# Performance work log

Measured on AMD Instinct MI355X. Metric: run time of the kernel, lower is better.

The kernel has to match this reference:

```python
import jax, jax.numpy as jnp
import numpy as np

EMBED_DIM = 1024

def setup_inputs() -> dict:
    key = jax.random.key(0)
    ks = jax.random.split(key, 7)
    D = EMBED_DIM
    x = jax.random.normal(ks[0], (4, 2048, D), dtype=jnp.float32)
    s = 1.0 / np.sqrt(D)
    Wq = jax.random.normal(ks[1], (D, D), dtype=jnp.float32) * s
    bq = jnp.zeros((D,), dtype=jnp.float32)
    Wk = jax.random.normal(ks[2], (D, D), dtype=jnp.float32) * s
    bk = jnp.zeros((D,), dtype=jnp.float32)
    Wv = jax.random.normal(ks[3], (D, D), dtype=jnp.float32) * s
    bv = jnp.zeros((D,), dtype=jnp.float32)
    return {"x": x, "Wq": Wq, "bq": bq, "Wk": Wk, "bk": bk, "Wv": Wv, "bv": bv}

def reference(x, Wq, bq, Wk, bk, Wv, bv):
    # x: [B,S,D]; torch Linear: x @ W.T + b -> here W is stored as [D_in, D_out]
    Q = jnp.einsum('bsd,de->bse', x, Wq) + bq
    K = jnp.einsum('bsd,de->bse', x, Wk) + bk
    V = jnp.einsum('bsd,de->bse', x, Wv) + bv
    scale = 1.0 / jnp.sqrt(jnp.asarray(x.shape[-1], dtype=x.dtype))
    scores = jnp.einsum('bqd,bkd->bqk', Q, K) * scale  # [B,S,S]
    probs = jax.nn.softmax(scores, axis=-1)
    # dropout is identity in eval mode
    return jnp.einsum('bqk,bkd->bqd', probs, V)
```

## Files before the change

### kernel.cpp

```cpp
#include <hip/hip_runtime.h>
#include <hip/hip_bf16.h>
#include <stdint.h>
#include <stddef.h>

#define D_EMB 1024
#define SEQ   2048
#define BATCH 4

typedef short bf16x8 __attribute__((ext_vector_type(8)));
typedef float f32x4  __attribute__((ext_vector_type(4)));

#define AS1 __attribute__((address_space(1)))
#define AS3 __attribute__((address_space(3)))

static __device__ __forceinline__ void async_copy16(const void* g, void* l) {
  __builtin_amdgcn_global_load_lds((const AS1 void*)g, (AS3 void*)l, 16, 0, 0);
}

static __device__ __forceinline__ void gemm128(
    const __hip_bfloat16* __restrict__ A, int lda,
    const __hip_bfloat16* __restrict__ Bt, int ldb,
    int K, f32x4 (&acc)[4][4])
{
  __shared__ __hip_bfloat16 ldsA[128 * 64];
  __shared__ __hip_bfloat16 ldsB[128 * 64];

  const int t    = threadIdx.x;
  const int wave = t >> 6;
  const int lane = t & 63;
  const int quad = lane >> 4;
  const int lr   = lane & 15;
  const int wr   = wave >> 1;
  const int wc   = wave & 1;

  const int r0 = t >> 3;
  const int c0 = (((t & 7) ^ (r0 & 7)) * 8);

  const __hip_bfloat16* gA = A  + (size_t)r0 * lda + c0;
  const __hip_bfloat16* gB = Bt + (size_t)r0 * ldb + c0;
  char* lA = (char*)ldsA + wave * 1024;
  char* lB = (char*)ldsB + wave * 1024;

  for (int k0 = 0; k0 < K; k0 += 64) {
    __syncthreads();
#pragma unroll
    for (int ch = 0; ch < 4; ch++) {
      async_copy16(gA + k0 + (size_t)(32 * ch) * lda, lA + 4096 * ch);
      async_copy16(gB + k0 + (size_t)(32 * ch) * ldb, lB + 4096 * ch);
    }
    __syncthreads();

#pragma unroll
    for (int kk = 0; kk < 64; kk += 32) {
      bf16x8 aF[4], bF[4];
      const int lc = (kk >> 3) + quad;
      const int pc = (lc ^ (lr & 7)) * 8;
#pragma unroll
      for (int i = 0; i < 4; i++)
        aF[i] = *(const bf16x8*)&ldsA[(wr * 64 + i * 16 + lr) * 64 + pc];
#pragma unroll
      for (int j = 0; j < 4; j++)
        bF[j] = *(const bf16x8*)&ldsB[(wc * 64 + j * 16 + lr) * 64 + pc];

#pragma unroll
      for (int i = 0; i < 4; i++)
#pragma unroll
        for (int j = 0; j < 4; j++)
          acc[i][j] = __builtin_amdgcn_mfma_f32_16x16x32_bf16(aF[i], bF[j], acc[i][j], 0, 0, 0);
    }
  }
}

#define ZERO_ACC(acc)                         \
  {                                           \
    f32x4 _z = {0.f, 0.f, 0.f, 0.f};          \
    _Pragma("unroll")                         \
    for (int _i = 0; _i < 4; _i++)            \
      _Pragma("unroll")                       \
      for (int _j = 0; _j < 4; _j++)          \
        acc[_i][_j] = _z;                     \
  }

__global__ __launch_bounds__(256) void convert_x(
    const float* __restrict__ x, __hip_bfloat16* __restrict__ xb)
{
  const size_t i = ((size_t)blockIdx.x * 256 + threadIdx.x) * 4;
  const float4 v = *(const float4*)(x + i);
  __hip_bfloat16 o[4] = {__float2bfloat16(v.x), __float2bfloat16(v.y),
                         __float2bfloat16(v.z), __float2bfloat16(v.w)};
  *(uint64_t*)(xb + i) = *(uint64_t*)o;
}

__global__ __launch_bounds__(256) void transpose_w3(
    const float* __restrict__ Wq,
    const float* __restrict__ Wk,
    const float* __restrict__ Wv,
    __hip_bfloat16* __restrict__ Wt3)
{
  const float* src = (blockIdx.z == 0) ? Wq : (blockIdx.z == 1) ? Wk : Wv;
  __hip_bfloat16* dst = Wt3 + (size_t)blockIdx.z * D_EMB * D_EMB;
  __shared__ __hip_bfloat16 tile[32][33];
  const int x0 = blockIdx.x * 32;
  const int y0 = blockIdx.y * 32;
  const int tx = threadIdx.x, ty = threadIdx.y;
#pragma unroll
  for (int i = 0; i < 32; i += 8)
    tile[ty + i][tx] = __float2bfloat16(src[(size_t)(y0 + ty + i) * D_EMB + (x0 + tx)]);
  __syncthreads();
#pragma unroll
  for (int i = 0; i < 32; i += 8)
    dst[(size_t)(x0 + ty + i) * D_EMB + (y0 + tx)] = tile[tx][ty + i];
}

__global__ __launch_bounds__(256) void qkv_kernel(
    const __hip_bfloat16* __restrict__ xb,
    const __hip_bfloat16* __restrict__ Wt3,
    const float* __restrict__ bq,
    const float* __restrict__ bk,
    const float* __restrict__ bv,
    __hip_bfloat16* __restrict__ Q,
    __hip_bfloat16* __restrict__ Kb,
    __hip_bfloat16* __restrict__ Vt)
{
  const int mat = blockIdx.z;
  const int m0  = blockIdx.x * 128;
  const int n0  = blockIdx.y * 128;

  f32x4 acc[4][4];
  ZERO_ACC(acc);

  gemm128(xb + (size_t)m0 * D_EMB, D_EMB,
          Wt3 + (size_t)mat * D_EMB * D_EMB + (size_t)n0 * D_EMB, D_EMB,
          D_EMB, acc);

  const float* bias = (mat == 0) ? bq : (mat == 1) ? bk : bv;

  const int t = threadIdx.x;
  const int wave = t >> 6, lane = t & 63;
  const int quad = lane >> 4, lr = lane & 15;
  const int wr = wave >> 1, wc = wave & 1;

#pragma unroll
  for (int i = 0; i < 4; i++) {
#pragma unroll
    for (int j = 0; j < 4; j++) {
      const int n = n0 + wc * 64 + j * 16 + lr;
      const float bb = bias[n];
#pragma unroll
      for (int r = 0; r < 4; r++) {
        const int m = m0 + wr * 64 + i * 16 + quad * 4 + r;
        const float v = acc[i][j][r] + bb;
        if (mat == 0) {
          Q[(size_t)m * D_EMB + n] = __float2bfloat16(v);
        } else if (mat == 1) {
          Kb[(size_t)m * D_EMB + n] = __float2bfloat16(v);
        } else {
          const int b = m >> 11, s = m & 2047;
          Vt[(size_t)b * D_EMB * SEQ + (size_t)n * SEQ + s] = __float2bfloat16(v);
        }
      }
    }
  }
}

__global__ __launch_bounds__(256) void scores_kernel(
    const __hip_bfloat16* __restrict__ Q,
    const __hip_bfloat16* __restrict__ Kb,
    float* __restrict__ Sc)
{
  const int b  = blockIdx.z;
  const int m0 = blockIdx.y * 128;
  const int n0 = blockIdx.x * 128;

  f32x4 acc[4][4];
  ZERO_ACC(acc);

  gemm128(Q  + (size_t)b * SEQ * D_EMB + (size_t)m0 * D_EMB, D_EMB,
          Kb + (size_t)b * SEQ * D_EMB + (size_t)n0 * D_EMB, D_EMB,
          D_EMB, acc);

  float* out = Sc + (size_t)b * SEQ * SEQ;
  const float scale = 0.03125f;

  const int t = threadIdx.x;
  const int wave = t >> 6, lane = t & 63;
  const int quad = lane >> 4, lr = lane & 15;
  const int wr = wave >> 1, wc = wave & 1;

#pragma unroll
  for (int i = 0; i < 4; i++)
#pragma unroll
    for (int j = 0; j < 4; j++) {
      const int n = n0 + wc * 64 + j * 16 + lr;
#pragma unroll
      for (int r = 0; r < 4; r++) {
        const int m = m0 + wr * 64 + i * 16 + quad * 4 + r;
        out[(size_t)m * SEQ + n] = acc[i][j][r] * scale;
      }
    }
}

__global__ __launch_bounds__(256) void softmax_kernel(
    const float* __restrict__ Sc, __hip_bfloat16* __restrict__ P)
{
  const int row = blockIdx.x;
  const float* src = Sc + (size_t)row * SEQ;
  const int t = threadIdx.x;
  const int wave = t >> 6, lane = t & 63;

  float v[8];
#pragma unroll
  for (int i = 0; i < 8; i++) v[i] = src[t + 256 * i];

  float m = v[0];
#pragma unroll
  for (int i = 1; i < 8; i++) m = fmaxf(m, v[i]);
#pragma unroll
  for (int o = 32; o > 0; o >>= 1) m = fmaxf(m, __shfl_xor(m, o));

  __shared__ float redm[4];
  __shared__ float reds[4];
  if (lane == 0) redm[wave] = m;
  __syncthreads();
  m = fmaxf(fmaxf(redm[0], redm[1]), fmaxf(redm[2], redm[3]));

  float e[8], s = 0.f;
#pragma unroll
  for (int i = 0; i < 8; i++) { e[i] = __expf(v[i] - m); s += e[i]; }
#pragma unroll
  for (int o = 32; o > 0; o >>= 1) s += __shfl_xor(s, o);
  if (lane == 0) reds[wave] = s;
  __syncthreads();
  s = reds[0] + reds[1] + reds[2] + reds[3];

  const float inv = 1.f / s;
  __hip_bfloat16* dst = P + (size_t)row * SEQ;
#pragma unroll
  for (int i = 0; i < 8; i++) dst[t + 256 * i] = __float2bfloat16(e[i] * inv);
}

__global__ __launch_bounds__(256) void pv_kernel(
    const __hip_bfloat16* __restrict__ P,
    const __hip_bfloat16* __restrict__ Vt,
    float* __restrict__ out)
{
  const int b  = blockIdx.z;
  const int m0 = blockIdx.y * 128;
  const int n0 = blockIdx.x * 128;

  f32x4 acc[4][4];
  ZERO_ACC(acc);

  gemm128(P  + (size_t)b * SEQ * SEQ   + (size_t)m0 * SEQ, SEQ,
          Vt + (size_t)b * D_EMB * SEQ + (size_t)n0 * SEQ, SEQ,
          SEQ, acc);

  float* o = out + (size_t)b * SEQ * D_EMB;

  const int t = threadIdx.x;
  const int wave = t >> 6, lane = t & 63;
  const int quad = lane >> 4, lr = lane & 15;
  const int wr = wave >> 1, wc = wave & 1;

#pragma unroll
  for (int i = 0; i < 4; i++)
#pragma unroll
    for (int j = 0; j < 4; j++) {
      const int n = n0 + wc * 64 + j * 16 + lr;
#pragma unroll
      for (int r = 0; r < 4; r++) {
        const int m = m0 + wr * 64 + i * 16 + quad * 4 + r;
        o[(size_t)m * D_EMB + n] = acc[i][j][r];
      }
    }
}

extern "C" void kernel_launch(void* const* d_in, const int* in_sizes, int n_in,
                              void* d_out, int out_size, void* d_ws, size_t ws_size,
                              hipStream_t stream) {
  const float* x  = (const float*)d_in[0];
  const float* Wq = (const float*)d_in[1];
  const float* bq = (const float*)d_in[2];
  const float* Wk = (const float*)d_in[3];
  const float* bk = (const float*)d_in[4];
  const float* Wv = (const float*)d_in[5];
  const float* bv = (const float*)d_in[6];
  float* out = (float*)d_out;

  char* ws = (char*)d_ws;
  __hip_bfloat16* xb  = (__hip_bfloat16*)(ws);
  __hip_bfloat16* Wt3 = (__hip_bfloat16*)(ws + 16777216);
  __hip_bfloat16* Q   = (__hip_bfloat16*)(ws + 23068672);
  __hip_bfloat16* Kb  = (__hip_bfloat16*)(ws + 39845888);
  __hip_bfloat16* Vt  = (__hip_bfloat16*)(ws + 56623104);
  float*          Sc  = (float*)         (ws + 73400320);
  __hip_bfloat16* P   = (__hip_bfloat16*)(ws + 140509184);

  convert_x    <<<dim3(8192),      256,        0, stream>>>(x, xb);
  transpose_w3 <<<dim3(32, 32, 3), dim3(32, 8), 0, stream>>>(Wq, Wk, Wv, Wt3);
  qkv_kernel   <<<dim3(64, 8, 3),  256,        0, stream>>>(xb, Wt3, bq, bk, bv, Q, Kb, Vt);
  scores_kernel<<<dim3(16, 16, 4), 256,        0, stream>>>(Q, Kb, Sc);
  softmax_kernel<<<dim3(8192),     256,        0, stream>>>(Sc, P);
  pv_kernel    <<<dim3(8, 16, 4),  256,        0, stream>>>(P, Vt, out);
}
```

Measured before the change: 282.7 us.

## Double-buffer GEMM LDS tiles, fp16 scores, fuse prep kernels, vectorize V stores

Result: faster. 269.3 us (-4.7%).

```diff
diff --git a/kernel.cpp b/kernel.cpp
--- a/kernel.cpp
+++ b/kernel.cpp
@@ -1,5 +1,6 @@
 #include <hip/hip_runtime.h>
 #include <hip/hip_bf16.h>
+#include <hip/hip_fp16.h>
 #include <stdint.h>
 #include <stddef.h>
 
@@ -22,8 +23,8 @@
     const __hip_bfloat16* __restrict__ Bt, int ldb,
     int K, f32x4 (&acc)[4][4])
 {
-  __shared__ __hip_bfloat16 ldsA[128 * 64];
-  __shared__ __hip_bfloat16 ldsB[128 * 64];
+  __shared__ __hip_bfloat16 ldsA[2][128 * 64];
+  __shared__ __hip_bfloat16 ldsB[2][128 * 64];
 
   const int t    = threadIdx.x;
   const int wave = t >> 6;
@@ -38,18 +39,36 @@
 
   const __hip_bfloat16* gA = A  + (size_t)r0 * lda + c0;
   const __hip_bfloat16* gB = Bt + (size_t)r0 * ldb + c0;
-  char* lA = (char*)ldsA + wave * 1024;
-  char* lB = (char*)ldsB + wave * 1024;
-
-  for (int k0 = 0; k0 < K; k0 += 64) {
+
+  const int niter = K >> 6;
+
+  {
+    char* lA = (char*)ldsA[0] + wave * 1024;
+    char* lB = (char*)ldsB[0] + wave * 1024;
+#pragma unroll
+    for (int ch = 0; ch < 4; ch++) {
+      async_copy16(gA + (size_t)(32 * ch) * lda, lA + 4096 * ch);
+      async_copy16(gB + (size_t)(32 * ch) * ldb, lB + 4096 * ch);
+    }
+  }
+
+  int buf = 0;
+  for (int it = 0; it < niter; ++it) {
     __syncthreads();
-#pragma unroll
-    for (int ch = 0; ch < 4; ch++) {
-      async_copy16(gA + k0 + (size_t)(32 * ch) * lda, lA + 4096 * ch);
-      async_copy16(gB + k0 + (size_t)(32 * ch) * ldb, lB + 4096 * ch);
-    }
-    __syncthreads();
-
+
+    if (it + 1 < niter) {
+      const int k0 = (it + 1) << 6;
+      char* lA = (char*)ldsA[buf ^ 1] + wave * 1024;
+      char* lB = (char*)ldsB[buf ^ 1] + wave * 1024;
+#pragma unroll
+      for (int ch = 0; ch < 4; ch++) {
+        async_copy16(gA + k0 + (size_t)(32 * ch) * lda, lA + 4096 * ch);
+        async_copy16(gB + k0 + (size_t)(32 * ch) * ldb, lB + 4096 * ch);
+      }
+    }
+
+    const __hip_bfloat16* bA = ldsA[buf];
+    const __hip_bfloat16* bB = ldsB[buf];
 #pragma unroll
     for (int kk = 0; kk < 64; kk += 32) {
       bf16x8 aF[4], bF[4];
@@ -57,10 +76,10 @@
       const int pc = (lc ^ (lr & 7)) * 8;
 #pragma unroll
       for (int i = 0; i < 4; i++)
-        aF[i] = *(const bf16x8*)&ldsA[(wr * 64 + i * 16 + lr) * 64 + pc];
+        aF[i] = *(const bf16x8*)&bA[(wr * 64 + i * 16 + lr) * 64 + pc];
 #pragma unroll
       for (int j = 0; j < 4; j++)
-        bF[j] = *(const bf16x8*)&ldsB[(wc * 64 + j * 16 + lr) * 64 + pc];
+        bF[j] = *(const bf16x8*)&bB[(wc * 64 + j * 16 + lr) * 64 + pc];
 
 #pragma unroll
       for (int i = 0; i < 4; i++)
@@ -68,6 +87,7 @@
         for (int j = 0; j < 4; j++)
           acc[i][j] = __builtin_amdgcn_mfma_f32_16x16x32_bf16(aF[i], bF[j], acc[i][j], 0, 0, 0);
     }
+    buf ^= 1;
   }
 }
 
@@ -81,28 +101,33 @@
         acc[_i][_j] = _z;                     \
   }
 
-__global__ __launch_bounds__(256) void convert_x(
-    const float* __restrict__ x, __hip_bfloat16* __restrict__ xb)
-{
-  const size_t i = ((size_t)blockIdx.x * 256 + threadIdx.x) * 4;
-  const float4 v = *(const float4*)(x + i);
-  __hip_bfloat16 o[4] = {__float2bfloat16(v.x), __float2bfloat16(v.y),
-                         __float2bfloat16(v.z), __float2bfloat16(v.w)};
-  *(uint64_t*)(xb + i) = *(uint64_t*)o;
-}
-
-__global__ __launch_bounds__(256) void transpose_w3(
+__global__ __launch_bounds__(256) void prep_kernel(
+    const float* __restrict__ x,
     const float* __restrict__ Wq,
     const float* __restrict__ Wk,
     const float* __restrict__ Wv,
+    __hip_bfloat16* __restrict__ xb,
     __hip_bfloat16* __restrict__ Wt3)
 {
+  const int tx = threadIdx.x, ty = threadIdx.y;
+  if (blockIdx.z == 3) {
+    const int tid = ty * 32 + tx;
+    const size_t base = ((size_t)blockIdx.y * 32 + blockIdx.x) * 8192;
+#pragma unroll
+    for (int p = 0; p < 8; p++) {
+      const size_t i = base + p * 1024 + tid * 4;
+      const float4 v = *(const float4*)(x + i);
+      __hip_bfloat16 o[4] = {__float2bfloat16(v.x), __float2bfloat16(v.y),
+                             __float2bfloat16(v.z), __float2bfloat16(v.w)};
+      *(uint64_t*)(xb + i) = *(uint64_t*)o;
+    }
+    return;
+  }
   const float* src = (blockIdx.z == 0) ? Wq : (blockIdx.z == 1) ? Wk : Wv;
   __hip_bfloat16* dst = Wt3 + (size_t)blockIdx.z * D_EMB * D_EMB;
   __shared__ __hip_bfloat16 tile[32][33];
   const int x0 = blockIdx.x * 32;
   const int y0 = blockIdx.y * 32;
-  const int tx = threadIdx.x, ty = threadIdx.y;
 #pragma unroll
   for (int i = 0; i < 32; i += 8)
     tile[ty + i][tx] = __float2bfloat16(src[(size_t)(y0 + ty + i) * D_EMB + (x0 + tx)]);
@@ -146,18 +171,18 @@
     for (int j = 0; j < 4; j++) {
       const int n = n0 + wc * 64 + j * 16 + lr;
       const float bb = bias[n];
-#pragma unroll
-      for (int r = 0; r < 4; r++) {
-        const int m = m0 + wr * 64 + i * 16 + quad * 4 + r;
-        const float v = acc[i][j][r] + bb;
-        if (mat == 0) {
-          Q[(size_t)m * D_EMB + n] = __float2bfloat16(v);
-        } else if (mat == 1) {
-          Kb[(size_t)m * D_EMB + n] = __float2bfloat16(v);
-        } else {
-          const int b = m >> 11, s = m & 2047;
-          Vt[(size_t)b * D_EMB * SEQ + (size_t)n * SEQ + s] = __float2bfloat16(v);
-        }
+      const int mbase = m0 + wr * 64 + i * 16 + quad * 4;
+      if (mat == 2) {
+        const int b = mbase >> 11, s = mbase & 2047;
+        __hip_bfloat16 pk[4];
+#pragma unroll
+        for (int r = 0; r < 4; r++) pk[r] = __float2bfloat16(acc[i][j][r] + bb);
+        *(uint64_t*)&Vt[(size_t)b * D_EMB * SEQ + (size_t)n * SEQ + s] = *(uint64_t*)pk;
+      } else {
+        __hip_bfloat16* dst = (mat == 0) ? Q : Kb;
+#pragma unroll
+        for (int r = 0; r < 4; r++)
+          dst[(size_t)(mbase + r) * D_EMB + n] = __float2bfloat16(acc[i][j][r] + bb);
       }
     }
   }
@@ -166,7 +191,7 @@
 __global__ __launch_bounds__(256) void scores_kernel(
     const __hip_bfloat16* __restrict__ Q,
     const __hip_bfloat16* __restrict__ Kb,
-    float* __restrict__ Sc)
+    __half* __restrict__ Sc)
 {
   const int b  = blockIdx.z;
   const int m0 = blockIdx.y * 128;
@@ -179,7 +204,7 @@
           Kb + (size_t)b * SEQ * D_EMB + (size_t)n0 * D_EMB, D_EMB,
           D_EMB, acc);
 
-  float* out = Sc + (size_t)b * SEQ * SEQ;
+  __half* out = Sc + (size_t)b * SEQ * SEQ;
   const float scale = 0.03125f;
 
   const int t = threadIdx.x;
@@ -195,22 +220,22 @@
 #pragma unroll
       for (int r = 0; r < 4; r++) {
         const int m = m0 + wr * 64 + i * 16 + quad * 4 + r;
-        out[(size_t)m * SEQ + n] = acc[i][j][r] * scale;
+        out[(size_t)m * SEQ + n] = __float2half(acc[i][j][r] * scale);
       }
     }
 }
 
 __global__ __launch_bounds__(256) void softmax_kernel(
-    const float* __restrict__ Sc, __hip_bfloat16* __restrict__ P)
+    const __half* __restrict__ Sc, __hip_bfloat16* __restrict__ P)
 {
   const int row = blockIdx.x;
-  const float* src = Sc + (size_t)row * SEQ;
+  const __half* src = Sc + (size_t)row * SEQ;
   const int t = threadIdx.x;
   const int wave = t >> 6, lane = t & 63;
 
   float v[8];
 #pragma unroll
-  for (int i = 0; i < 8; i++) v[i] = src[t + 256 * i];
+  for (int i = 0; i < 8; i++) v[i] = __half2float(src[t + 256 * i]);
 
   float m = v[0];
 #pragma unroll
@@ -293,11 +318,10 @@
   __hip_bfloat16* Q   = (__hip_bfloat16*)(ws + 23068672);
   __hip_bfloat16* Kb  = (__hip_bfloat16*)(ws + 39845888);
   __hip_bfloat16* Vt  = (__hip_bfloat16*)(ws + 56623104);
-  float*          Sc  = (float*)         (ws + 73400320);
+  __half*         Sc  = (__half*)        (ws + 73400320);
   __hip_bfloat16* P   = (__hip_bfloat16*)(ws + 140509184);
 
-  convert_x    <<<dim3(8192),      256,        0, stream>>>(x, xb);
-  transpose_w3 <<<dim3(32, 32, 3), dim3(32, 8), 0, stream>>>(Wq, Wk, Wv, Wt3);
+  prep_kernel  <<<dim3(32, 32, 4), dim3(32, 8), 0, stream>>>(x, Wq, Wk, Wv, xb, Wt3);
   qkv_kernel   <<<dim3(64, 8, 3),  256,        0, stream>>>(xb, Wt3, bq, bk, bv, Q, Kb, Vt);
   scores_kernel<<<dim3(16, 16, 4), 256,        0, stream>>>(Q, Kb, Sc);
   softmax_kernel<<<dim3(8192),     256,        0, stream>>>(Sc, P);
```
